# Kernel tuning notes

Hardware: AMD Instinct MI355X
Metric: run time of the kernel (lower is better)

## Reference

```python
import jax, jax.numpy as jnp
import numpy as np

C = 8      # num_channels
H = 512    # dim_hidden
B, S = 32, 1024
EPS = 1e-5


def _layernorm(x, gamma, beta):
    mu = jnp.mean(x, axis=-1, keepdims=True)
    var = jnp.var(x, axis=-1, keepdims=True)
    return (x - mu) * jax.lax.rsqrt(var + EPS) * gamma + beta


def setup_inputs() -> dict:
    key = jax.random.key(0)
    ks = jax.random.split(key, 7)
    x = jax.random.normal(ks[0], (C, B, S, 1), dtype=jnp.float32)
    # per-channel Linear(1,H): torch weight [H,1] -> stacked as [C,H]
    enc_w = jax.random.normal(ks[1], (C, H), dtype=jnp.float32) / jnp.sqrt(1.0)
    enc_b = jax.random.normal(ks[2], (C, H), dtype=jnp.float32) * 0.02
    enc_gamma = jnp.ones((C, H), dtype=jnp.float32)
    enc_beta = jnp.zeros((C, H), dtype=jnp.float32)
    # modulator Linear(C*H -> H): torch weight [H, C*H]
    mod_w = jax.random.normal(ks[3], (H, C * H), dtype=jnp.float32) / jnp.sqrt(C * H)
    mod_b = jax.random.normal(ks[4], (H,), dtype=jnp.float32) * 0.02
    mod_gamma = jnp.ones((H,), dtype=jnp.float32)
    mod_beta = jnp.zeros((H,), dtype=jnp.float32)
    return {
        "x": x,
        "enc_w": enc_w, "enc_b": enc_b,
        "enc_gamma": enc_gamma, "enc_beta": enc_beta,
        "mod_w": mod_w, "mod_b": mod_b,
        "mod_gamma": mod_gamma, "mod_beta": mod_beta,
    }


def reference(x, enc_w, enc_b, enc_gamma, enc_beta, mod_w, mod_b, mod_gamma, mod_beta):
    # per-channel Linear(1,H): h[c,b,s,:] = x[c,b,s,0]*enc_w[c] + enc_b[c]
    h = x * enc_w[:, None, None, :] + enc_b[:, None, None, :]      # [C,B,S,H]
    h = _layernorm(h, enc_gamma[:, None, None, :], enc_beta[:, None, None, :])
    h = jax.nn.gelu(h, approximate=False)
    # concat along last dim in channel order -> [B,S,C*H]
    h = jnp.transpose(h, (1, 2, 0, 3)).reshape(B, S, C * H)
    # channel modulator: Linear + LayerNorm + GELU
    y = jnp.einsum("bsk,hk->bsh", h, mod_w) + mod_b                # [B,S,H]
    y = _layernorm(y, mod_gamma, mod_beta)
    return jax.nn.gelu(y, approximate=False)
```

## Files before the change

### kernel.cpp

```cpp
#include <hip/hip_runtime.h>
#include <hip/hip_bf16.h>
#include <math.h>

#define C_CH 8
#define H_DIM 512
#define BS 32768
#define K_DIM 4096
#define EPS 1e-5f

#define TM 64
#define TK 32
#define NKT (K_DIM / TK)
#define GRP 4
#define NGRP (NKT / GRP)
#define AELEMS (TM * TK * GRP)

typedef __bf16 bf16x8 __attribute__((ext_vector_type(8)));
typedef float  floatx16 __attribute__((ext_vector_type(16)));

__device__ __forceinline__ float gelu_fast(float v) {
    float x2 = v * fmaf(v * v, 0.102943215f, 2.30220815f);
    float e = __builtin_amdgcn_exp2f(-x2);
    return v * __builtin_amdgcn_rcpf(1.0f + e);
}

__global__ __launch_bounds__(256) void prep_kernel(
    const float* __restrict__ w, __bf16* __restrict__ o,
    const float* __restrict__ enc_w, const float* __restrict__ enc_b,
    const float* __restrict__ enc_gamma,
    float* __restrict__ Wf, float* __restrict__ Bf, float* __restrict__ st)
{
    __shared__ float red[4][5];
    if (blockIdx.x < 1024) {
        int gtid  = blockIdx.x * 256 + threadIdx.x;
        int lane  = gtid & 63;
        int chunk = gtid >> 6;
        int kh    = chunk >> 4;
        int n32   = chunk & 15;
        int col   = n32 * 32 + (lane & 31);
        int k     = kh * 16 + (lane >> 5) * 8;
        const float* src = w + (size_t)col * K_DIM + k;
        float4 a = *(const float4*)src;
        float4 b = *(const float4*)(src + 4);
        bf16x8 h;
        h[0] = (__bf16)a.x; h[1] = (__bf16)a.y; h[2] = (__bf16)a.z; h[3] = (__bf16)a.w;
        h[4] = (__bf16)b.x; h[5] = (__bf16)b.y; h[6] = (__bf16)b.z; h[7] = (__bf16)b.w;
        *(bf16x8*)(o + (size_t)gtid * 8) = h;
    } else {
        const int c = blockIdx.x - 1024;
        const int t = threadIdx.x;
        const float* wp = enc_w + c * H_DIM;
        const float* bp = enc_b + c * H_DIM;
        const float* gp = enc_gamma + c * H_DIM;
        float w0 = wp[t], w1 = wp[t + 256];
        float b0 = bp[t], b1 = bp[t + 256];
        float sw  = w0 + w1;
        float sb  = b0 + b1;
        float sww = fmaf(w0, w0, w1 * w1);
        float sbb = fmaf(b0, b0, b1 * b1);
        float swb = fmaf(w0, b0, w1 * b1);
        #pragma unroll
        for (int off = 32; off; off >>= 1) {
            sw  += __shfl_xor(sw,  off);
            sb  += __shfl_xor(sb,  off);
            sww += __shfl_xor(sww, off);
            sbb += __shfl_xor(sbb, off);
            swb += __shfl_xor(swb, off);
        }
        int wv = t >> 6, ln = t & 63;
        if (ln == 0) {
            red[wv][0] = sw;  red[wv][1] = sb;  red[wv][2] = sww;
            red[wv][3] = sbb; red[wv][4] = swb;
        }
        __syncthreads();
        float tsw  = red[0][0] + red[1][0] + red[2][0] + red[3][0];
        float tsb  = red[0][1] + red[1][1] + red[2][1] + red[3][1];
        float tsww = red[0][2] + red[1][2] + red[2][2] + red[3][2];
        float tsbb = red[0][3] + red[1][3] + red[2][3] + red[3][3];
        float tswb = red[0][4] + red[1][4] + red[2][4] + red[3][4];
        const float inv = 1.0f / (float)H_DIM;
        float mw = tsw * inv, mb = tsb * inv;
        if (t == 0) {
            st[c * 4 + 0] = tsww * inv - mw * mw;
            st[c * 4 + 1] = 2.0f * (tswb * inv - mw * mb);
            st[c * 4 + 2] = tsbb * inv - mb * mb;
        }
        float g0 = gp[t], g1 = gp[t + 256];
        Wf[c * H_DIM + t]       = g0 * (w0 - mw);
        Wf[c * H_DIM + t + 256] = g1 * (w1 - mw);
        Bf[c * H_DIM + t]       = g0 * (b0 - mb);
        Bf[c * H_DIM + t + 256] = g1 * (b1 - mb);
    }
}

template <int USE_WS>
__global__ __launch_bounds__(512, 4) void fused_gemm_kernel(
    const float* __restrict__ x,
    const float* __restrict__ enc_w,
    const float* __restrict__ enc_b,
    const float* __restrict__ enc_gamma,
    const float* __restrict__ enc_beta,
    const float* __restrict__ mod_w,
    const __bf16* __restrict__ Wb,
    const float* __restrict__ Wf,
    const float* __restrict__ Bf,
    const float* __restrict__ st,
    const float* __restrict__ mod_b,
    const float* __restrict__ mod_gamma,
    const float* __restrict__ mod_beta,
    float* __restrict__ out)
{
    __shared__ float stats[C_CH][5];
    __shared__ float pS[C_CH][TM];
    __shared__ float qS[C_CH][TM];
    __shared__ float rS[C_CH][TM];
    __shared__ __align__(16) __bf16 Als[2 * AELEMS];
    __shared__ float redS[TM][8];
    __shared__ float redQ[TM][8];
    __shared__ float muS[TM];
    __shared__ float invS[TM];

    const int tid  = threadIdx.x;
    const int wave = tid >> 6;
    const int lane = tid & 63;
    const int row0 = blockIdx.x * TM;

    if (USE_WS) {
        int c = wave;
        int m = lane;
        float xv = x[c * BS + row0 + m];
        float vw = st[c * 4 + 0], cwb2 = st[c * 4 + 1], vb = st[c * 4 + 2];
        float q = rsqrtf(fmaf(xv, fmaf(xv, vw, cwb2), vb) + EPS);
        pS[c][m] = xv * q;
        qS[c][m] = q;
    } else {
        {
            const int c = wave;
            float sw = 0.f, sb = 0.f, sww = 0.f, sbb = 0.f, swb = 0.f;
            for (int j = lane; j < H_DIM; j += 64) {
                float w = enc_w[c * H_DIM + j];
                float b = enc_b[c * H_DIM + j];
                sw += w; sb += b;
                sww = fmaf(w, w, sww);
                sbb = fmaf(b, b, sbb);
                swb = fmaf(w, b, swb);
            }
            #pragma unroll
            for (int off = 32; off; off >>= 1) {
                sw  += __shfl_xor(sw,  off);
                sb  += __shfl_xor(sb,  off);
                sww += __shfl_xor(sww, off);
                sbb += __shfl_xor(sbb, off);
                swb += __shfl_xor(swb, off);
            }
            if (lane == 0) {
                const float inv = 1.0f / (float)H_DIM;
                float mw = sw * inv, mb = sb * inv;
                stats[c][0] = mw;
                stats[c][1] = mb;
                stats[c][2] = sww * inv - mw * mw;
                stats[c][3] = sbb * inv - mb * mb;
                stats[c][4] = swb * inv - mw * mb;
            }
        }
        __syncthreads();
        {
            int c = wave;
            int m = lane;
            float xv = x[c * BS + row0 + m];
            float mw = stats[c][0], mb = stats[c][1];
            float vw = stats[c][2], vb = stats[c][3], cwb = stats[c][4];
            float var = fmaf(xv, fmaf(xv, vw, 2.0f * cwb), vb);
            float q = rsqrtf(var + EPS);
            float p = xv * q;
            pS[c][m] = p;
            qS[c][m] = q;
            rS[c][m] = -fmaf(p, mw, q * mb);
        }
    }
    __syncthreads();

    const int wn = wave;

    const int scg   = tid >> 6;
    const int sq    = scg & 3;
    const int skh   = sq >> 1;
    const int smt   = sq & 1;
    const int sl    = tid & 63;
    const int skoff = skh * 16 + (sl >> 5) * 8;
    const int arow  = smt * 32 + (sl & 31);
    const int ssub0 = scg >> 2;
    const int sdst0 = (sq * 512) + sl * 8;

    floatx16 acc[2][2];
    #pragma unroll
    for (int i = 0; i < 2; ++i)
        #pragma unroll
        for (int j = 0; j < 2; ++j)
            #pragma unroll
            for (int r = 0; r < 16; ++r)
                acc[i][j][r] = 0.f;

    auto stageSlot = [&](int g1, int which, __bf16* dstbuf, float p, float q) {
        const int sub = ssub0 + which * 2;
        const int k0  = (g1 * GRP + sub) * TK + skoff;
        float4 w0 = *(const float4*)(Wf + k0);
        float4 w1 = *(const float4*)(Wf + k0 + 4);
        float4 b0 = *(const float4*)(Bf + k0);
        float4 b1 = *(const float4*)(Bf + k0 + 4);
        float4 e0 = *(const float4*)(enc_beta + k0);
        float4 e1 = *(const float4*)(enc_beta + k0 + 4);
        float fw[8] = {w0.x, w0.y, w0.z, w0.w, w1.x, w1.y, w1.z, w1.w};
        float fb[8] = {b0.x, b0.y, b0.z, b0.w, b1.x, b1.y, b1.z, b1.w};
        float fe[8] = {e0.x, e0.y, e0.z, e0.w, e1.x, e1.y, e1.z, e1.w};
        bf16x8 hv;
        #pragma unroll
        for (int i = 0; i < 8; ++i) {
            float v = fmaf(p, fw[i], fmaf(q, fb[i], fe[i]));
            hv[i] = (__bf16)gelu_fast(v);
        }
        *(bf16x8*)(dstbuf + sub * 2048 + sdst0) = hv;
    };

    auto stageSlotL = [&](int g1, int which, __bf16* dstbuf,
                          float p, float q, float r) {
        const int sub = ssub0 + which * 2;
        const int k0  = (g1 * GRP + sub) * TK + skoff;
        float4 w0 = *(const float4*)(enc_w + k0);
        float4 w1 = *(const float4*)(enc_w + k0 + 4);
        float4 b0 = *(const float4*)(enc_b + k0);
        float4 b1 = *(const float4*)(enc_b + k0 + 4);
        float4 g0 = *(const float4*)(enc_gamma + k0);
        float4 g1v = *(const float4*)(enc_gamma + k0 + 4);
        float4 e0 = *(const float4*)(enc_beta + k0);
        float4 e1 = *(const float4*)(enc_beta + k0 + 4);
        float fw[8] = {w0.x, w0.y, w0.z, w0.w, w1.x, w1.y, w1.z, w1.w};
        float fb[8] = {b0.x, b0.y, b0.z, b0.w, b1.x, b1.y, b1.z, b1.w};
        float fg[8] = {g0.x, g0.y, g0.z, g0.w, g1v.x, g1v.y, g1v.z, g1v.w};
        float fe[8] = {e0.x, e0.y, e0.z, e0.w, e1.x, e1.y, e1.z, e1.w};
        bf16x8 hv;
        #pragma unroll
        for (int i = 0; i < 8; ++i) {
            float t = fmaf(p, fw[i], fmaf(q, fb[i], r));
            float v = fmaf(t, fg[i], fe[i]);
            hv[i] = (__bf16)gelu_fast(v);
        }
        *(bf16x8*)(dstbuf + sub * 2048 + sdst0) = hv;
    };

    const __bf16* baseB = Wb + (size_t)(wn * 128 + lane) * 8;
    auto loadB = [&](int kt, int half, bf16x8* dst) {
        if (USE_WS) {
            const __bf16* bp = baseB + (size_t)(2 * kt + half) * 8192;
            dst[0] = *(const bf16x8*)bp;
            dst[1] = *(const bf16x8*)(bp + 512);
        } else {
            const int k = (2 * kt + half) * 16 + (lane >> 5) * 8;
            #pragma unroll
            for (int nt = 0; nt < 2; ++nt) {
                int col = (wn * 2 + nt) * 32 + (lane & 31);
                const float* src = mod_w + (size_t)col * K_DIM + k;
                float4 a = *(const float4*)src;
                float4 b = *(const float4*)(src + 4);
                bf16x8 h;
                h[0] = (__bf16)a.x; h[1] = (__bf16)a.y; h[2] = (__bf16)a.z; h[3] = (__bf16)a.w;
                h[4] = (__bf16)b.x; h[5] = (__bf16)b.y; h[6] = (__bf16)b.z; h[7] = (__bf16)b.w;
                dst[nt] = h;
            }
        }
    };

    bf16x8 bfrP[2], bfrQ[2];
    loadB(0, 0, bfrP);
    if (USE_WS) {
        float p0 = pS[0][arow], q0 = qS[0][arow];
        stageSlot(0, 0, Als, p0, q0);
        stageSlot(0, 1, Als, p0, q0);
    } else {
        float p0 = pS[0][arow], q0 = qS[0][arow], r0 = rS[0][arow];
        stageSlotL(0, 0, Als, p0, q0, r0);
        stageSlotL(0, 1, Als, p0, q0, r0);
    }
    __syncthreads();

    for (int g = 0; g < NGRP; ++g) {
        __bf16* cur = Als + (g & 1) * AELEMS;
        __bf16* nxt = Als + ((g + 1) & 1) * AELEMS;
        const bool haveNext = (g + 1 < NGRP);

        float pC = 0.f, qC = 0.f, rC = 0.f;
        if (haveNext) {
            const int cn = (g + 1) >> 2;
            pC = pS[cn][arow];
            qC = qS[cn][arow];
            if (!USE_WS) rC = rS[cn][arow];
        }

        #pragma unroll
        for (int sub = 0; sub < GRP; ++sub) {
            const int kt = g * GRP + sub;

            loadB(kt, 1, bfrQ);

            if (haveNext && sub == 0) {
                if (USE_WS) stageSlot(g + 1, 0, nxt, pC, qC);
                else        stageSlotL(g + 1, 0, nxt, pC, qC, rC);
            }
            if (haveNext && sub == 2) {
                if (USE_WS) stageSlot(g + 1, 1, nxt, pC, qC);
                else        stageSlotL(g + 1, 1, nxt, pC, qC, rC);
            }

            const __bf16* Acur = cur + sub * (TM * TK);
            bf16x8 af[2][2];
            #pragma unroll
            for (int kh = 0; kh < 2; ++kh)
                #pragma unroll
                for (int mt = 0; mt < 2; ++mt)
                    af[kh][mt] = *(const bf16x8*)(Acur + (kh * 2 + mt) * 512 + lane * 8);

            __builtin_amdgcn_s_setprio(1);
            #pragma unroll
            for (int mt = 0; mt < 2; ++mt)
                #pragma unroll
                for (int nt = 0; nt < 2; ++nt)
                    acc[mt][nt] = __builtin_amdgcn_mfma_f32_32x32x16_bf16(
                        af[0][mt], bfrP[nt], acc[mt][nt], 0, 0, 0);
            __builtin_amdgcn_s_setprio(0);

            if (kt + 1 < NKT) loadB(kt + 1, 0, bfrP);

            __builtin_amdgcn_s_setprio(1);
            #pragma unroll
            for (int mt = 0; mt < 2; ++mt)
                #pragma unroll
                for (int nt = 0; nt < 2; ++nt)
                    acc[mt][nt] = __builtin_amdgcn_mfma_f32_32x32x16_bf16(
                        af[1][mt], bfrQ[nt], acc[mt][nt], 0, 0, 0);
            __builtin_amdgcn_s_setprio(0);
        }
        __syncthreads();
    }

    float mbv[2], gv[2], bev[2];
    #pragma unroll
    for (int nt = 0; nt < 2; ++nt) {
        int col = wn * 64 + nt * 32 + (lane & 31);
        mbv[nt] = mod_b[col];
        gv[nt]  = mod_gamma[col];
        bev[nt] = mod_beta[col];
    }
    #pragma unroll
    for (int mt = 0; mt < 2; ++mt)
        #pragma unroll
        for (int nt = 0; nt < 2; ++nt)
            #pragma unroll
            for (int r = 0; r < 16; ++r)
                acc[mt][nt][r] += mbv[nt];

    #pragma unroll
    for (int mt = 0; mt < 2; ++mt) {
        #pragma unroll
        for (int r = 0; r < 16; ++r) {
            float y0 = acc[mt][0][r];
            float y1 = acc[mt][1][r];
            float s  = y0 + y1;
            float ss = fmaf(y0, y0, y1 * y1);
            #pragma unroll
            for (int off = 1; off < 32; off <<= 1) {
                s  += __shfl_xor(s,  off);
                ss += __shfl_xor(ss, off);
            }
            if ((lane & 31) == 0) {
                int row = mt * 32 + (r & 3) + ((r >> 2) << 3) + ((lane >> 5) << 2);
                redS[row][wn] = s;
                redQ[row][wn] = ss;
            }
        }
    }
    __syncthreads();
    if (tid < TM) {
        float s = 0.f, ss = 0.f;
        #pragma unroll
        for (int w = 0; w < 8; ++w) {
            s  += redS[tid][w];
            ss += redQ[tid][w];
        }
        const float inv_n = 1.0f / (float)H_DIM;
        float mu  = s * inv_n;
        float var = ss * inv_n - mu * mu;
        muS[tid]  = mu;
        invS[tid] = rsqrtf(var + EPS);
    }
    __syncthreads();

    #pragma unroll
    for (int mt = 0; mt < 2; ++mt) {
        #pragma unroll
        for (int r = 0; r < 16; ++r) {
            int row = mt * 32 + (r & 3) + ((r >> 2) << 3) + ((lane >> 5) << 2);
            float mu  = muS[row];
            float inv = invS[row];
            float* op = out + (size_t)(row0 + row) * H_DIM;
            #pragma unroll
            for (int nt = 0; nt < 2; ++nt) {
                int col = wn * 64 + nt * 32 + (lane & 31);
                float t = fmaf((acc[mt][nt][r] - mu) * inv, gv[nt], bev[nt]);
                op[col] = gelu_fast(t);
            }
        }
    }
}

extern "C" void kernel_launch(void* const* d_in, const int* in_sizes, int n_in,
                              void* d_out, int out_size, void* d_ws, size_t ws_size,
                              hipStream_t stream) {
    const float* x         = (const float*)d_in[0];
    const float* enc_w     = (const float*)d_in[1];
    const float* enc_b     = (const float*)d_in[2];
    const float* enc_gamma = (const float*)d_in[3];
    const float* enc_beta  = (const float*)d_in[4];
    const float* mod_w     = (const float*)d_in[5];
    const float* mod_b     = (const float*)d_in[6];
    const float* mod_gamma = (const float*)d_in[7];
    const float* mod_beta  = (const float*)d_in[8];
    float* out = (float*)d_out;

    const size_t wb_bytes = (size_t)H_DIM * K_DIM * sizeof(__bf16);
    const size_t wf_off   = wb_bytes;
    const size_t bf_off   = wf_off + (size_t)C_CH * H_DIM * sizeof(float);
    const size_t st_off   = bf_off + (size_t)C_CH * H_DIM * sizeof(float);
    const size_t need     = st_off + (size_t)C_CH * 4 * sizeof(float);

    int use_ws = (ws_size >= need) ? 1 : 0;
    __bf16* Wb = (__bf16*)d_ws;
    float*  Wf = (float*)((char*)d_ws + wf_off);
    float*  Bf = (float*)((char*)d_ws + bf_off);
    float*  st = (float*)((char*)d_ws + st_off);

    if (use_ws) {
        prep_kernel<<<1024 + C_CH, 256, 0, stream>>>(
            mod_w, Wb, enc_w, enc_b, enc_gamma, Wf, Bf, st);
        fused_gemm_kernel<1><<<BS / TM, 512, 0, stream>>>(
            x, enc_w, enc_b, enc_gamma, enc_beta, mod_w, Wb, Wf, Bf, st,
            mod_b, mod_gamma, mod_beta, out);
    } else {
        fused_gemm_kernel<0><<<BS / TM, 512, 0, stream>>>(
            x, enc_w, enc_b, enc_gamma, enc_beta, mod_w, Wb,
            (const float*)0, (const float*)0, (const float*)0,
            mod_b, mod_gamma, mod_beta, out);
    }
}
```

Measured before the change: 270.0 us.

## Halve row tile and switch to 16x16x32 MFMA with deeper B prefetch

Shrinks the block row tile from 64 to 32, which doubles the number of blocks, and replaces the 32x32x16 MFMAs with 16x16x32 MFMAs. The prepacked bf16 weight layout is reorganised to match the new fragment shape. B fragments are now prefetched two k-steps ahead using four register sets, and each group is staged in a single call with a lighter waitcnt+barrier. The intent is more parallelism and better latency hiding, at the cost of half as much A-tile reuse and twice as much weight traffic per output row.

```diff
diff --git a/kernel.cpp b/kernel.cpp
--- a/kernel.cpp
+++ b/kernel.cpp
@@ -8,7 +8,7 @@
 #define K_DIM 4096
 #define EPS 1e-5f
 
-#define TM 64
+#define TM 32
 #define TK 32
 #define NKT (K_DIM / TK)
 #define GRP 4
@@ -16,7 +16,7 @@
 #define AELEMS (TM * TK * GRP)
 
 typedef __bf16 bf16x8 __attribute__((ext_vector_type(8)));
-typedef float  floatx16 __attribute__((ext_vector_type(16)));
+typedef float  floatx4 __attribute__((ext_vector_type(4)));
 
 __device__ __forceinline__ float gelu_fast(float v) {
     float x2 = v * fmaf(v * v, 0.102943215f, 2.30220815f);
@@ -35,10 +35,10 @@
         int gtid  = blockIdx.x * 256 + threadIdx.x;
         int lane  = gtid & 63;
         int chunk = gtid >> 6;
-        int kh    = chunk >> 4;
-        int n32   = chunk & 15;
-        int col   = n32 * 32 + (lane & 31);
-        int k     = kh * 16 + (lane >> 5) * 8;
+        int kt    = chunk >> 5;
+        int ntile = chunk & 31;
+        int col   = ntile * 16 + (lane & 15);
+        int k     = kt * 32 + (lane >> 4) * 8;
         const float* src = w + (size_t)col * K_DIM + k;
         float4 a = *(const float4*)src;
         float4 b = *(const float4*)(src + 4);
@@ -114,7 +114,7 @@
     __shared__ float pS[C_CH][TM];
     __shared__ float qS[C_CH][TM];
     __shared__ float rS[C_CH][TM];
-    __shared__ __align__(16) __bf16 Als[2 * AELEMS];
+    __shared__ __align__(16) __bf16 Als[2][AELEMS];
     __shared__ float redS[TM][8];
     __shared__ float redQ[TM][8];
     __shared__ float muS[TM];
@@ -123,23 +123,54 @@
     const int tid  = threadIdx.x;
     const int wave = tid >> 6;
     const int lane = tid & 63;
+    const int lr   = lane & 15;
+    const int lq   = lane >> 4;
     const int row0 = blockIdx.x * TM;
 
+    const __bf16* baseB = Wb + ((size_t)(wave * 4) * 64 + lane) * 8;
+    auto loadB = [&](int kt, int j, bf16x8 (&dst)[2]) {
+        if (USE_WS) {
+            const __bf16* bp = baseB + ((size_t)kt * 32 + j * 2) * 512;
+            dst[0] = *(const bf16x8*)bp;
+            dst[1] = *(const bf16x8*)(bp + 512);
+        } else {
+            const int kk = kt * 32 + lq * 8;
+            #pragma unroll
+            for (int n2 = 0; n2 < 2; ++n2) {
+                int col = wave * 64 + (j * 2 + n2) * 16 + lr;
+                const float* src = mod_w + (size_t)col * K_DIM + kk;
+                float4 a = *(const float4*)src;
+                float4 b = *(const float4*)(src + 4);
+                bf16x8 h;
+                h[0] = (__bf16)a.x; h[1] = (__bf16)a.y; h[2] = (__bf16)a.z; h[3] = (__bf16)a.w;
+                h[4] = (__bf16)b.x; h[5] = (__bf16)b.y; h[6] = (__bf16)b.z; h[7] = (__bf16)b.w;
+                dst[n2] = h;
+            }
+        }
+    };
+
+    bf16x8 rA[2], rB[2], rC[2], rD[2];
+    loadB(0, 0, rA);
+    loadB(0, 1, rB);
+    loadB(1, 0, rC);
+    loadB(1, 1, rD);
+
     if (USE_WS) {
-        int c = wave;
-        int m = lane;
-        float xv = x[c * BS + row0 + m];
-        float vw = st[c * 4 + 0], cwb2 = st[c * 4 + 1], vb = st[c * 4 + 2];
-        float q = rsqrtf(fmaf(xv, fmaf(xv, vw, cwb2), vb) + EPS);
-        pS[c][m] = xv * q;
-        qS[c][m] = q;
+        if (tid < C_CH * TM) {
+            int c = tid >> 5, m = tid & 31;
+            float xv = x[c * BS + row0 + m];
+            float vw = st[c * 4 + 0], cwb2 = st[c * 4 + 1], vb = st[c * 4 + 2];
+            float q = rsqrtf(fmaf(xv, fmaf(xv, vw, cwb2), vb) + EPS);
+            pS[c][m] = xv * q;
+            qS[c][m] = q;
+        }
     } else {
         {
             const int c = wave;
             float sw = 0.f, sb = 0.f, sww = 0.f, sbb = 0.f, swb = 0.f;
-            for (int j = lane; j < H_DIM; j += 64) {
-                float w = enc_w[c * H_DIM + j];
-                float b = enc_b[c * H_DIM + j];
+            for (int jj = lane; jj < H_DIM; jj += 64) {
+                float w = enc_w[c * H_DIM + jj];
+                float b = enc_b[c * H_DIM + jj];
                 sw += w; sb += b;
                 sww = fmaf(w, w, sww);
                 sbb = fmaf(b, b, sbb);
@@ -164,9 +195,8 @@
             }
         }
         __syncthreads();
-        {
-            int c = wave;
-            int m = lane;
+        if (tid < C_CH * TM) {
+            int c = tid >> 5, m = tid & 31;
             float xv = x[c * BS + row0 + m];
             float mw = stats[c][0], mb = stats[c][1];
             float vw = stats[c][2], vb = stats[c][3], cwb = stats[c][4];
@@ -180,30 +210,17 @@
     }
     __syncthreads();
 
-    const int wn = wave;
-
-    const int scg   = tid >> 6;
-    const int sq    = scg & 3;
-    const int skh   = sq >> 1;
-    const int smt   = sq & 1;
+    const int ssub  = tid >> 7;
+    const int smt   = (tid >> 6) & 1;
     const int sl    = tid & 63;
-    const int skoff = skh * 16 + (sl >> 5) * 8;
-    const int arow  = smt * 32 + (sl & 31);
-    const int ssub0 = scg >> 2;
-    const int sdst0 = (sq * 512) + sl * 8;
-
-    floatx16 acc[2][2];
-    #pragma unroll
-    for (int i = 0; i < 2; ++i)
-        #pragma unroll
-        for (int j = 0; j < 2; ++j)
-            #pragma unroll
-            for (int r = 0; r < 16; ++r)
-                acc[i][j][r] = 0.f;
-
-    auto stageSlot = [&](int g1, int which, __bf16* dstbuf, float p, float q) {
-        const int sub = ssub0 + which * 2;
-        const int k0  = (g1 * GRP + sub) * TK + skoff;
+    const int srow  = smt * 16 + (sl & 15);
+    const int skk   = ssub * TK + (sl >> 4) * 8;
+    const int sdoff = (ssub * 2 + smt) * 512 + sl * 8;
+
+    auto stageGroup = [&](int g1, __bf16* dstbuf) {
+        const int c = g1 >> 2;
+        const float p = pS[c][srow], q = qS[c][srow];
+        const int k0 = g1 * 128 + skk;
         float4 w0 = *(const float4*)(Wf + k0);
         float4 w1 = *(const float4*)(Wf + k0 + 4);
         float4 b0 = *(const float4*)(Bf + k0);
@@ -219,13 +236,13 @@
             float v = fmaf(p, fw[i], fmaf(q, fb[i], fe[i]));
             hv[i] = (__bf16)gelu_fast(v);
         }
-        *(bf16x8*)(dstbuf + sub * 2048 + sdst0) = hv;
+        *(bf16x8*)(dstbuf + sdoff) = hv;
     };
 
-    auto stageSlotL = [&](int g1, int which, __bf16* dstbuf,
-                          float p, float q, float r) {
-        const int sub = ssub0 + which * 2;
-        const int k0  = (g1 * GRP + sub) * TK + skoff;
+    auto stageGroupL = [&](int g1, __bf16* dstbuf) {
+        const int c = g1 >> 2;
+        const float p = pS[c][srow], q = qS[c][srow], r = rS[c][srow];
+        const int k0 = g1 * 128 + skk;
         float4 w0 = *(const float4*)(enc_w + k0);
         float4 w1 = *(const float4*)(enc_w + k0 + 4);
         float4 b0 = *(const float4*)(enc_b + k0);
@@ -245,107 +262,66 @@
             float v = fmaf(t, fg[i], fe[i]);
             hv[i] = (__bf16)gelu_fast(v);
         }
-        *(bf16x8*)(dstbuf + sub * 2048 + sdst0) = hv;
+        *(bf16x8*)(dstbuf + sdoff) = hv;
     };
 
-    const __bf16* baseB = Wb + (size_t)(wn * 128 + lane) * 8;
-    auto loadB = [&](int kt, int half, bf16x8* dst) {
-        if (USE_WS) {
-            const __bf16* bp = baseB + (size_t)(2 * kt + half) * 8192;
-            dst[0] = *(const bf16x8*)bp;
-            dst[1] = *(const bf16x8*)(bp + 512);
-        } else {
-            const int k = (2 * kt + half) * 16 + (lane >> 5) * 8;
-            #pragma unroll
-            for (int nt = 0; nt < 2; ++nt) {
-                int col = (wn * 2 + nt) * 32 + (lane & 31);
-                const float* src = mod_w + (size_t)col * K_DIM + k;
-                float4 a = *(const float4*)src;
-                float4 b = *(const float4*)(src + 4);
-                bf16x8 h;
-                h[0] = (__bf16)a.x; h[1] = (__bf16)a.y; h[2] = (__bf16)a.z; h[3] = (__bf16)a.w;
-                h[4] = (__bf16)b.x; h[5] = (__bf16)b.y; h[6] = (__bf16)b.z; h[7] = (__bf16)b.w;
-                dst[nt] = h;
-            }
-        }
+    floatx4 acc[2][4];
+    #pragma unroll
+    for (int i = 0; i < 2; ++i)
+        #pragma unroll
+        for (int j = 0; j < 4; ++j)
+            acc[i][j] = (floatx4){0.f, 0.f, 0.f, 0.f};
+
+    auto mfmaSub = [&](const __bf16* Acur, int sub, int kt,
+                       bf16x8 (&sE)[2], bf16x8 (&sO)[2]) {
+        bf16x8 af0 = *(const bf16x8*)(Acur + (sub * 2 + 0) * 512 + lane * 8);
+        bf16x8 af1 = *(const bf16x8*)(Acur + (sub * 2 + 1) * 512 + lane * 8);
+        __builtin_amdgcn_s_setprio(1);
+        acc[0][0] = __builtin_amdgcn_mfma_f32_16x16x32_bf16(af0, sE[0], acc[0][0], 0, 0, 0);
+        acc[1][0] = __builtin_amdgcn_mfma_f32_16x16x32_bf16(af1, sE[0], acc[1][0], 0, 0, 0);
+        acc[0][1] = __builtin_amdgcn_mfma_f32_16x16x32_bf16(af0, sE[1], acc[0][1], 0, 0, 0);
+        acc[1][1] = __builtin_amdgcn_mfma_f32_16x16x32_bf16(af1, sE[1], acc[1][1], 0, 0, 0);
+        __builtin_amdgcn_s_setprio(0);
+        if (kt + 2 < NKT) loadB(kt + 2, 0, sE);
+        __builtin_amdgcn_s_setprio(1);
+        acc[0][2] = __builtin_amdgcn_mfma_f32_16x16x32_bf16(af0, sO[0], acc[0][2], 0, 0, 0);
+        acc[1][2] = __builtin_amdgcn_mfma_f32_16x16x32_bf16(af1, sO[0], acc[1][2], 0, 0, 0);
+        acc[0][3] = __builtin_amdgcn_mfma_f32_16x16x32_bf16(af0, sO[1], acc[0][3], 0, 0, 0);
+        acc[1][3] = __builtin_amdgcn_mfma_f32_16x16x32_bf16(af1, sO[1], acc[1][3], 0, 0, 0);
+        __builtin_amdgcn_s_setprio(0);
+        if (kt + 2 < NKT) loadB(kt + 2, 1, sO);
     };
 
-    bf16x8 bfrP[2], bfrQ[2];
-    loadB(0, 0, bfrP);
-    if (USE_WS) {
-        float p0 = pS[0][arow], q0 = qS[0][arow];
-        stageSlot(0, 0, Als, p0, q0);
-        stageSlot(0, 1, Als, p0, q0);
-    } else {
-        float p0 = pS[0][arow], q0 = qS[0][arow], r0 = rS[0][arow];
-        stageSlotL(0, 0, Als, p0, q0, r0);
-        stageSlotL(0, 1, Als, p0, q0, r0);
-    }
-    __syncthreads();
+    if (USE_WS) stageGroup(0, &Als[0][0]);
+    else        stageGroupL(0, &Als[0][0]);
+    asm volatile("s_waitcnt lgkmcnt(0)" ::: "memory");
+    __builtin_amdgcn_s_barrier();
+    __builtin_amdgcn_sched_barrier(0);
 
     for (int g = 0; g < NGRP; ++g) {
-        __bf16* cur = Als + (g & 1) * AELEMS;
-        __bf16* nxt = Als + ((g + 1) & 1) * AELEMS;
-        const bool haveNext = (g + 1 < NGRP);
-
-        float pC = 0.f, qC = 0.f, rC = 0.f;
-        if (haveNext) {
-            const int cn = (g + 1) >> 2;
-            pC = pS[cn][arow];
-            qC = qS[cn][arow];
-            if (!USE_WS) rC = rS[cn][arow];
-        }
-
-        #pragma unroll
-        for (int sub = 0; sub < GRP; ++sub) {
-            const int kt = g * GRP + sub;
-
-            loadB(kt, 1, bfrQ);
-
-            if (haveNext && sub == 0) {
-                if (USE_WS) stageSlot(g + 1, 0, nxt, pC, qC);
-                else        stageSlotL(g + 1, 0, nxt, pC, qC, rC);
-            }
-            if (haveNext && sub == 2) {
-                if (USE_WS) stageSlot(g + 1, 1, nxt, pC, qC);
-                else        stageSlotL(g + 1, 1, nxt, pC, qC, rC);
-            }
-
-            const __bf16* Acur = cur + sub * (TM * TK);
-            bf16x8 af[2][2];
-            #pragma unroll
-            for (int kh = 0; kh < 2; ++kh)
-                #pragma unroll
-                for (int mt = 0; mt < 2; ++mt)
-                    af[kh][mt] = *(const bf16x8*)(Acur + (kh * 2 + mt) * 512 + lane * 8);
-
-            __builtin_amdgcn_s_setprio(1);
-            #pragma unroll
-            for (int mt = 0; mt < 2; ++mt)
-                #pragma unroll
-                for (int nt = 0; nt < 2; ++nt)
-                    acc[mt][nt] = __builtin_amdgcn_mfma_f32_32x32x16_bf16(
-                        af[0][mt], bfrP[nt], acc[mt][nt], 0, 0, 0);
-            __builtin_amdgcn_s_setprio(0);
-
-            if (kt + 1 < NKT) loadB(kt + 1, 0, bfrP);
-
-            __builtin_amdgcn_s_setprio(1);
-            #pragma unroll
-            for (int mt = 0; mt < 2; ++mt)
-                #pragma unroll
-                for (int nt = 0; nt < 2; ++nt)
-                    acc[mt][nt] = __builtin_amdgcn_mfma_f32_32x32x16_bf16(
-                        af[1][mt], bfrQ[nt], acc[mt][nt], 0, 0, 0);
-            __builtin_amdgcn_s_setprio(0);
-        }
-        __syncthreads();
-    }
-
-    float mbv[2], gv[2], bev[2];
+        const __bf16* cur = &Als[g & 1][0];
+        __bf16*       nxt = &Als[(g + 1) & 1][0];
+        const int kt0 = g * GRP;
+
+        if (g + 1 < NGRP) {
+            if (USE_WS) stageGroup(g + 1, nxt);
+            else        stageGroupL(g + 1, nxt);
+        }
+
+        mfmaSub(cur, 0, kt0 + 0, rA, rB);
+        mfmaSub(cur, 1, kt0 + 1, rC, rD);
+        mfmaSub(cur, 2, kt0 + 2, rA, rB);
+        mfmaSub(cur, 3, kt0 + 3, rC, rD);
+
+        asm volatile("s_waitcnt lgkmcnt(0)" ::: "memory");
+        __builtin_amdgcn_s_barrier();
+        __builtin_amdgcn_sched_barrier(0);
+    }
+
+    float mbv[4], gv[4], bev[4];
     #pragma unroll
-    for (int nt = 0; nt < 2; ++nt) {
-        int col = wn * 64 + nt * 32 + (lane & 31);
+    for (int nt = 0; nt < 4; ++nt) {
+        int col = wave * 64 + nt * 16 + lr;
         mbv[nt] = mod_b[col];
         gv[nt]  = mod_gamma[col];
         bev[nt] = mod_beta[col];
@@ -353,28 +329,31 @@
     #pragma unroll
     for (int mt = 0; mt < 2; ++mt)
         #pragma unroll
-        for (int nt = 0; nt < 2; ++nt)
-            #pragma unroll
-            for (int r = 0; r < 16; ++r)
+        for (int nt = 0; nt < 4; ++nt)
+            #pragma unroll
+            for (int r = 0; r < 4; ++r)
                 acc[mt][nt][r] += mbv[nt];
 
     #pragma unroll
     for (int mt = 0; mt < 2; ++mt) {
         #pragma unroll
-        for (int r = 0; r < 16; ++r) {
-            float y0 = acc[mt][0][r];
-            float y1 = acc[mt][1][r];
-            float s  = y0 + y1;
-            float ss = fmaf(y0, y0, y1 * y1);
-            #pragma unroll
-            for (int off = 1; off < 32; off <<= 1) {
+        for (int r = 0; r < 4; ++r) {
+            float s = 0.f, ss = 0.f;
+            #pragma unroll
+            for (int nt = 0; nt < 4; ++nt) {
+                float y = acc[mt][nt][r];
+                s += y;
+                ss = fmaf(y, y, ss);
+            }
+            #pragma unroll
+            for (int off = 1; off < 16; off <<= 1) {
                 s  += __shfl_xor(s,  off);
                 ss += __shfl_xor(ss, off);
             }
-            if ((lane & 31) == 0) {
-                int row = mt * 32 + (r & 3) + ((r >> 2) << 3) + ((lane >> 5) << 2);
-                redS[row][wn] = s;
-                redQ[row][wn] = ss;
+            if (lr == 0) {
+                int row = mt * 16 + lq * 4 + r;
+                redS[row][wave] = s;
+                redQ[row][wave] = ss;
             }
         }
     }
@@ -397,14 +376,14 @@
     #pragma unroll
     for (int mt = 0; mt < 2; ++mt) {
         #pragma unroll
-        for (int r = 0; r < 16; ++r) {
-            int row = mt * 32 + (r & 3) + ((r >> 2) << 3) + ((lane >> 5) << 2);
+        for (int r = 0; r < 4; ++r) {
+            int row = mt * 16 + lq * 4 + r;
             float mu  = muS[row];
             float inv = invS[row];
             float* op = out + (size_t)(row0 + row) * H_DIM;
             #pragma unroll
-            for (int nt = 0; nt < 2; ++nt) {
-                int col = wn * 64 + nt * 32 + (lane & 31);
+            for (int nt = 0; nt < 4; ++nt) {
+                int col = wave * 64 + nt * 16 + lr;
                 float t = fmaf((acc[mt][nt][r] - mu) * inv, gv[nt], bev[nt]);
                 op[col] = gelu_fast(t);
             }
```

Result: slower. 277.8 us (+2.9%).
